# Performance work log

Hardware: AMD Instinct MI355X
Metric: run time of the kernel (lower is better)

The kernel has to match this reference:

```python
import jax, jax.numpy as jnp
import numpy as np

B, L, D = 2, 1024, 1024
HID, E, K = 2048, 8, 2

def setup_inputs() -> dict:
    key = jax.random.key(0)
    ks = jax.random.split(key, 4)
    std = 0.02
    return {
        "x": jax.random.normal(ks[0], (B, L, D), dtype=jnp.float32),
        "router_scale": jnp.ones((D,), dtype=jnp.float32),
        "router_w": jax.random.normal(ks[1], (D, E), dtype=jnp.float32) * std,
        "gating_w": jax.random.normal(ks[2], (E, 2, HID, D), dtype=jnp.float32) * std,
        "linear_w": jax.random.normal(ks[3], (E, HID, D), dtype=jnp.float32) * std,
        "per_expert_scale": jnp.ones((E,), dtype=jnp.float32),
    }

def reference(x, router_scale, router_w, gating_w, linear_w, per_expert_scale):
    d = x.shape[-1]
    # RMSNorm without scale
    var = jnp.mean(jnp.square(x), axis=-1, keepdims=True)
    r_in = x * jax.lax.rsqrt(var + 1e-6)
    r_in = r_in * jax.lax.rsqrt(jnp.array(d, dtype=r_in.dtype)) * router_scale
    # Router
    logits = jnp.dot(r_in, router_w).astype(jnp.float32)          # [B,L,E]
    probs = jax.nn.softmax(logits, axis=-1)
    _, top_k_idx = jax.lax.top_k(logits, K)                        # [B,L,K]
    indicator = jax.nn.one_hot(top_k_idx, probs.shape[-1], dtype=probs.dtype)  # [B,L,K,E]
    gate_weights = indicator.sum(axis=-2) * probs                  # [B,L,E]
    renorm = jnp.sum(gate_weights, axis=-1, keepdims=True)
    renorm = jnp.where(renorm > 0.0, renorm, 1.0)
    weights = probs / renorm
    top_k_w = jnp.take_along_axis(weights, top_k_idx, axis=-1)     # [B,L,K]
    # Combine weights per expert (indices in top-k are distinct)
    combine = jnp.einsum('blke,blk->ble', indicator, top_k_w)      # [B,L,E]
    combine = combine * per_expert_scale                            # fold per-expert scale
    # Dense all-expert GELU-gated FFN; identical math to per-token gathered weights,
    # since unselected experts get combine weight 0.
    gate0 = jnp.einsum('bld,ehd->bleh', x, gating_w[:, 0])         # [B,L,E,H]
    gate1 = jnp.einsum('bld,ehd->bleh', x, gating_w[:, 1])
    act = jax.nn.gelu(gate0) * gate1                               # approximate gelu, as flax nn.gelu
    out = jnp.einsum('bleh,ehd,ble->bld', act, linear_w, combine)
    return out.astype(x.dtype)
```

## Files before the change

### kernel.cpp

```cpp
#include <hip/hip_runtime.h>
#include <math.h>

#define NB 2
#define NL 1024
#define ND 1024
#define NH 2048
#define NE 8
#define NTOK (NB*NL)
#define NSLOT (NTOK*2)

typedef float f32x4 __attribute__((ext_vector_type(4)));
typedef short s16x8 __attribute__((ext_vector_type(8)));
typedef short s16x4 __attribute__((ext_vector_type(4)));

struct TokMeta { int i0, i1; float w0, w1; };

__device__ __forceinline__ unsigned short f2bf(float f) {
    union { float f; unsigned u; } v; v.f = f;
    unsigned r = v.u + 0x7FFFu + ((v.u >> 16) & 1u);
    return (unsigned short)(r >> 16);
}

__global__ void router_kernel(const float* __restrict__ x,
                              const float* __restrict__ rscale,
                              const float* __restrict__ rw,
                              const float* __restrict__ pes,
                              int* __restrict__ counts,
                              TokMeta* __restrict__ meta)
{
    const int wave = threadIdx.x >> 6;
    const int lane = threadIdx.x & 63;
    const int t = blockIdx.x * 4 + wave;
    const float* xt = x + (size_t)t * ND;

    float part[NE];
#pragma unroll
    for (int e = 0; e < NE; ++e) part[e] = 0.f;
    float ss = 0.f;

#pragma unroll
    for (int i = 0; i < 4; ++i) {
        int d = (lane + 64 * i) * 4;
        float4 xv = *(const float4*)(xt + d);
        float4 sv = *(const float4*)(rscale + d);
        float xs[4] = {xv.x, xv.y, xv.z, xv.w};
        float sc[4] = {sv.x, sv.y, sv.z, sv.w};
        const float* rwp = rw + (size_t)d * NE;
#pragma unroll
        for (int c = 0; c < 4; ++c) {
            float v = xs[c];
            ss += v * v;
            float xr = v * sc[c];
            float4 r0 = *(const float4*)(rwp + c * NE);
            float4 r1 = *(const float4*)(rwp + c * NE + 4);
            part[0] += xr * r0.x; part[1] += xr * r0.y;
            part[2] += xr * r0.z; part[3] += xr * r0.w;
            part[4] += xr * r1.x; part[5] += xr * r1.y;
            part[6] += xr * r1.z; part[7] += xr * r1.w;
        }
    }
#pragma unroll
    for (int off = 32; off > 0; off >>= 1) {
        ss += __shfl_xor(ss, off, 64);
#pragma unroll
        for (int e = 0; e < NE; ++e) part[e] += __shfl_xor(part[e], off, 64);
    }
    if (lane == 0) {
        float rinv = rsqrtf(ss * (1.f / ND) + 1e-6f) * rsqrtf((float)ND);
        float lg[NE];
#pragma unroll
        for (int e = 0; e < NE; ++e) lg[e] = part[e] * rinv;
        int i0 = 0; float b0 = lg[0];
#pragma unroll
        for (int e = 1; e < NE; ++e) if (lg[e] > b0) { b0 = lg[e]; i0 = e; }
        int i1 = -1; float b1 = -INFINITY;
#pragma unroll
        for (int e = 0; e < NE; ++e) if (e != i0 && lg[e] > b1) { b1 = lg[e]; i1 = e; }
        float e1 = expf(b1 - b0);
        float denom = 1.f + e1;
        float w0 = pes[i0] / denom;
        float w1 = pes[i1] * e1 / denom;
        meta[t].i0 = i0; meta[t].i1 = i1; meta[t].w0 = w0; meta[t].w1 = w1;
        atomicAdd(&counts[i0], 1);
        atomicAdd(&counts[i1], 1);
    }
}

__global__ void scan_kernel(const int* __restrict__ counts,
                            int* __restrict__ cursor, int* __restrict__ base)
{
    if (threadIdx.x == 0) {
        int acc = 0;
        for (int e = 0; e < NE; ++e) { base[e] = acc; cursor[e] = acc; acc += counts[e]; }
    }
}

__global__ void scatter_kernel(const TokMeta* __restrict__ meta, int* __restrict__ cursor,
                               int* __restrict__ tok_slot, float* __restrict__ w_slot)
{
    int t = blockIdx.x * blockDim.x + threadIdx.x;
    if (t >= NTOK) return;
    TokMeta m = meta[t];
    int s0 = atomicAdd(&cursor[m.i0], 1);
    tok_slot[s0] = t; w_slot[s0] = m.w0;
    int s1 = atomicAdd(&cursor[m.i1], 1);
    tok_slot[s1] = t; w_slot[s1] = m.w1;
}

__global__ __launch_bounds__(256) void gather_x(const float* __restrict__ x,
                                                const int* __restrict__ tok_slot,
                                                unsigned short* __restrict__ xg)
{
    const int s = blockIdx.x;
    const int tok = tok_slot[s];
    const int c = threadIdx.x * 4;
    float4 v = *(const float4*)(x + (size_t)tok * ND + c);
    s16x4 o;
    o[0] = (short)f2bf(v.x); o[1] = (short)f2bf(v.y);
    o[2] = (short)f2bf(v.z); o[3] = (short)f2bf(v.w);
    *(s16x4*)(xg + (size_t)s * ND + c) = o;
}

__global__ __launch_bounds__(256) void transpose_lw(const float* __restrict__ lw,
                                                    unsigned short* __restrict__ lwT)
{
    const int e = blockIdx.z;
    const int h0 = blockIdx.y * 64;
    const int d0 = blockIdx.x * 64;
    __shared__ unsigned short T[64][66];

    const int tid = threadIdx.x;
    {
        const int hr = tid >> 2;
        const int dc = (tid & 3) * 16;
        const float* p = lw + ((size_t)e * NH + h0 + hr) * ND + d0 + dc;
        float t[16];
        *(float4*)&t[0]  = *(const float4*)(p);
        *(float4*)&t[4]  = *(const float4*)(p + 4);
        *(float4*)&t[8]  = *(const float4*)(p + 8);
        *(float4*)&t[12] = *(const float4*)(p + 12);
#pragma unroll
        for (int i = 0; i < 8; ++i) {
            unsigned pk = (unsigned)f2bf(t[2 * i]) | ((unsigned)f2bf(t[2 * i + 1]) << 16);
            *(unsigned*)&T[hr][dc + 2 * i] = pk;
        }
    }
    __syncthreads();
    {
        const int dr = tid >> 2;
        const int hc = (tid & 3) * 16;
        s16x8 o0, o1;
#pragma unroll
        for (int i = 0; i < 8; ++i) o0[i] = (short)T[hc + i][dr];
#pragma unroll
        for (int i = 0; i < 8; ++i) o1[i] = (short)T[hc + 8 + i][dr];
        unsigned short* q = lwT + ((size_t)e * ND + d0 + dr) * NH + h0 + hc;
        *(s16x8*)(q)     = o0;
        *(s16x8*)(q + 8) = o1;
    }
}

#define BM 128
#define BH 64
#define BK 32
__global__ __launch_bounds__(256, 2) void gate_gemm(
    const unsigned short* __restrict__ xg, const float* __restrict__ gw,
    const int* __restrict__ base, const int* __restrict__ counts,
    const float* __restrict__ w_slot, unsigned short* __restrict__ act)
{
    const int e = blockIdx.z;
    const int n = counts[e];
    const int row0 = blockIdx.y * BM;
    if (row0 >= n) return;
    const int b0 = base[e];
    const int h0 = blockIdx.x * BH;

    __shared__ unsigned short As[BM][BK];
    __shared__ unsigned short Bs[2][BH][BK];
    __shared__ float swv[BM];

    const int tid = threadIdx.x;
    if (tid < BM) {
        int r = row0 + tid;
        swv[tid] = (r < n) ? w_slot[b0 + r] : 0.f;
    }

    const int lane = tid & 63;
    const int wid  = tid >> 6;
    const int wm = wid & 1;
    const int wn = wid >> 1;
    const int srow = tid >> 1;
    const int kh   = tid & 1;

    const bool arow_ok = (row0 + srow) < n;
    const unsigned short* xa = xg + (size_t)(b0 + row0 + srow) * ND + kh * 16;
    const int g  = srow >> 6;
    const int hh = srow & 63;
    const float* ba = gw + (((size_t)e * 2 + g) * NH + (h0 + hh)) * ND + kh * 16;

    f32x4 acc[2][4][2];
#pragma unroll
    for (int gg = 0; gg < 2; ++gg)
#pragma unroll
        for (int i = 0; i < 4; ++i)
#pragma unroll
            for (int j = 0; j < 2; ++j)
                acc[gg][i][j] = (f32x4){0.f, 0.f, 0.f, 0.f};

    const int fr = lane & 15;
    const int q8 = (lane >> 4) << 3;

    for (int k0 = 0; k0 < ND; k0 += BK) {
        s16x8 a0 = (s16x8)0, a1 = (s16x8)0;
        if (arow_ok) {
            a0 = *(const s16x8*)(xa + k0);
            a1 = *(const s16x8*)(xa + k0 + 8);
        }
        float t[16];
        *(float4*)&t[0]  = *(const float4*)(ba + k0);
        *(float4*)&t[4]  = *(const float4*)(ba + k0 + 4);
        *(float4*)&t[8]  = *(const float4*)(ba + k0 + 8);
        *(float4*)&t[12] = *(const float4*)(ba + k0 + 12);
        s16x8 b0v, b1v;
#pragma unroll
        for (int i = 0; i < 8; ++i) { b0v[i] = (short)f2bf(t[i]); b1v[i] = (short)f2bf(t[8 + i]); }

        *(s16x8*)&As[srow][kh * 16]      = a0;
        *(s16x8*)&As[srow][kh * 16 + 8]  = a1;
        *(s16x8*)&Bs[g][hh][kh * 16]     = b0v;
        *(s16x8*)&Bs[g][hh][kh * 16 + 8] = b1v;
        __syncthreads();

        s16x8 af[4], bfr[2][2];
#pragma unroll
        for (int i = 0; i < 4; ++i)
            af[i] = *(const s16x8*)&As[wm * 64 + i * 16 + fr][q8];
#pragma unroll
        for (int gg = 0; gg < 2; ++gg)
#pragma unroll
            for (int j = 0; j < 2; ++j)
                bfr[gg][j] = *(const s16x8*)&Bs[gg][wn * 32 + j * 16 + fr][q8];
#pragma unroll
        for (int gg = 0; gg < 2; ++gg)
#pragma unroll
            for (int i = 0; i < 4; ++i)
#pragma unroll
                for (int j = 0; j < 2; ++j)
                    acc[gg][i][j] = __builtin_amdgcn_mfma_f32_16x16x32_bf16(
                        af[i], bfr[gg][j], acc[gg][i][j], 0, 0, 0);
        __syncthreads();
    }

    const int rb = (lane >> 4) * 4;
#pragma unroll
    for (int i = 0; i < 4; ++i)
#pragma unroll
        for (int r = 0; r < 4; ++r) {
            int ml = wm * 64 + i * 16 + rb + r;
            int rr = row0 + ml;
            if (rr < n) {
                float w = swv[ml];
#pragma unroll
                for (int j = 0; j < 2; ++j) {
                    float g0v = acc[0][i][j][r];
                    float g1v = acc[1][i][j][r];
                    float u = 0.7978845608028654f * (g0v + 0.044715f * g0v * g0v * g0v);
                    float ex = __expf(2.f * u);
                    float th = 1.f - 2.f / (ex + 1.f);
                    float a = 0.5f * g0v * (1.f + th) * g1v * w;
                    act[(size_t)(b0 + rr) * NH + (h0 + wn * 32 + j * 16 + fr)] = f2bf(a);
                }
            }
        }
}

#define DBM 128
#define DBN 128
#define DBK 32
#define KSPLIT 2
#define KC (NH / KSPLIT)
__global__ __launch_bounds__(256, 2) void down_gemm(
    const unsigned short* __restrict__ act, const unsigned short* __restrict__ lwT,
    const int* __restrict__ base, const int* __restrict__ counts,
    const int* __restrict__ tok_slot, float* __restrict__ out)
{
    const int e  = blockIdx.z >> 1;
    const int kc = blockIdx.z & 1;
    const int n = counts[e];
    const int row0 = blockIdx.y * DBM;
    if (row0 >= n) return;
    const int b0 = base[e];
    const int d0 = blockIdx.x * DBN;

    __shared__ unsigned short As[DBM][DBK];
    __shared__ unsigned short Bs[DBN][DBK];
    __shared__ int stok[DBM];

    const int tid = threadIdx.x;
    if (tid < DBM) {
        int r = row0 + tid;
        stok[tid] = (r < n) ? tok_slot[b0 + r] : 0;
    }

    const int lane = tid & 63;
    const int wid  = tid >> 6;
    const int wm = wid & 1;
    const int wn = wid >> 1;
    const int srow = tid >> 1;
    const int kh   = tid & 1;

    const bool arow_ok = (row0 + srow) < n;
    const unsigned short* aa = act + (size_t)(b0 + row0 + srow) * NH + kc * KC + kh * 16;
    const unsigned short* bb = lwT + ((size_t)e * ND + d0 + srow) * NH + kc * KC + kh * 16;

    f32x4 acc[4][4];
#pragma unroll
    for (int i = 0; i < 4; ++i)
#pragma unroll
        for (int j = 0; j < 4; ++j)
            acc[i][j] = (f32x4){0.f, 0.f, 0.f, 0.f};

    const int fr = lane & 15;
    const int q8 = (lane >> 4) << 3;

    for (int k0 = 0; k0 < KC; k0 += DBK) {
        s16x8 a0 = (s16x8)0, a1 = (s16x8)0;
        if (arow_ok) {
            a0 = *(const s16x8*)(aa + k0);
            a1 = *(const s16x8*)(aa + k0 + 8);
        }
        s16x8 bv0 = *(const s16x8*)(bb + k0);
        s16x8 bv1 = *(const s16x8*)(bb + k0 + 8);

        *(s16x8*)&As[srow][kh * 16]     = a0;
        *(s16x8*)&As[srow][kh * 16 + 8] = a1;
        *(s16x8*)&Bs[srow][kh * 16]     = bv0;
        *(s16x8*)&Bs[srow][kh * 16 + 8] = bv1;
        __syncthreads();

        s16x8 af[4], bfr[4];
#pragma unroll
        for (int i = 0; i < 4; ++i)
            af[i] = *(const s16x8*)&As[wm * 64 + i * 16 + fr][q8];
#pragma unroll
        for (int j = 0; j < 4; ++j)
            bfr[j] = *(const s16x8*)&Bs[wn * 64 + j * 16 + fr][q8];
#pragma unroll
        for (int i = 0; i < 4; ++i)
#pragma unroll
            for (int j = 0; j < 4; ++j)
                acc[i][j] = __builtin_amdgcn_mfma_f32_16x16x32_bf16(af[i], bfr[j], acc[i][j], 0, 0, 0);
        __syncthreads();
    }

    const int rb = (lane >> 4) * 4;
#pragma unroll
    for (int i = 0; i < 4; ++i)
#pragma unroll
        for (int r = 0; r < 4; ++r) {
            int ml = wm * 64 + i * 16 + rb + r;
            int rr = row0 + ml;
            if (rr < n) {
                int tok = stok[ml];
#pragma unroll
                for (int j = 0; j < 4; ++j)
                    atomicAdd(&out[(size_t)tok * ND + d0 + wn * 64 + j * 16 + fr],
                              acc[i][j][r]);
            }
        }
}

extern "C" void kernel_launch(void* const* d_in, const int* in_sizes, int n_in,
                              void* d_out, int out_size, void* d_ws, size_t ws_size,
                              hipStream_t stream)
{
    const float* x      = (const float*)d_in[0];
    const float* rscale = (const float*)d_in[1];
    const float* rw     = (const float*)d_in[2];
    const float* gw     = (const float*)d_in[3];
    const float* lw     = (const float*)d_in[4];
    const float* pes    = (const float*)d_in[5];
    float* out = (float*)d_out;

    char* ws = (char*)d_ws;
    int* counts = (int*)ws;
    int* cursor = counts + 8;
    int* base   = counts + 16;
    TokMeta* meta        = (TokMeta*)(ws + 128);
    int*   tok_slot      = (int*)(ws + 33024);
    float* w_slot        = (float*)(ws + 49408);
    unsigned short* xg   = (unsigned short*)(ws + 65792);
    unsigned short* act  = (unsigned short*)(ws + 8454400);
    unsigned short* lwT  = (unsigned short*)(ws + 25231616);

    hipMemsetAsync(d_ws, 0, 128, stream);
    hipMemsetAsync(d_out, 0, (size_t)out_size * sizeof(float), stream);

    router_kernel<<<NTOK / 4, 256, 0, stream>>>(x, rscale, rw, pes, counts, meta);
    scan_kernel<<<1, 64, 0, stream>>>(counts, cursor, base);
    scatter_kernel<<<NTOK / 256, 256, 0, stream>>>(meta, cursor, tok_slot, w_slot);
    gather_x<<<NSLOT, 256, 0, stream>>>(x, tok_slot, xg);

    dim3 gt(ND / 64, NH / 64, NE);
    transpose_lw<<<gt, 256, 0, stream>>>(lw, lwT);

    dim3 g2(NH / BH, NTOK / BM, NE);
    gate_gemm<<<g2, 256, 0, stream>>>(xg, gw, base, counts, w_slot, act);

    dim3 g3(ND / DBN, NTOK / DBM, NE * KSPLIT);
    down_gemm<<<g3, 256, 0, stream>>>(act, lwT, base, counts, tok_slot, out);
}
```

Baseline: 461.4 us.

## Use direct global-to-LDS loads with swizzle and pre-converted bf16 gate weights

Both expert GEMMs now stage their tiles with global_load_lds (direct global-to-shared copies) and read fragments through an XOR-style swizzled column index, replacing register round-trips and bank-conflicting LDS reads. The gate weights are converted to bf16 once in a separate pass instead of being converted inside every gate_gemm tile. The per-slot x gather is replaced by a dense bf16 conversion of x, with rows gathered by token index inside the GEMM. The extra conversion pass over the gate weights adds a full read and write of that tensor each call. Out-of-range rows now load token 0 or slot 0 instead of zeros, which relies on the epilogue masking them out.

```diff
diff --git a/kernel.cpp b/kernel.cpp
--- a/kernel.cpp
+++ b/kernel.cpp
@@ -19,6 +19,12 @@
     union { float f; unsigned u; } v; v.f = f;
     unsigned r = v.u + 0x7FFFu + ((v.u >> 16) & 1u);
     return (unsigned short)(r >> 16);
+}
+
+__device__ __forceinline__ void gl_lds16(const unsigned short* g, unsigned short* l) {
+    __builtin_amdgcn_global_load_lds(
+        (const __attribute__((address_space(1))) unsigned int*)(const void*)g,
+        (__attribute__((address_space(3))) unsigned int*)(void*)l, 16, 0, 0);
 }
 
 __global__ void router_kernel(const float* __restrict__ x,
@@ -107,18 +113,30 @@
     tok_slot[s1] = t; w_slot[s1] = m.w1;
 }
 
-__global__ __launch_bounds__(256) void gather_x(const float* __restrict__ x,
-                                                const int* __restrict__ tok_slot,
-                                                unsigned short* __restrict__ xg)
-{
-    const int s = blockIdx.x;
-    const int tok = tok_slot[s];
-    const int c = threadIdx.x * 4;
-    float4 v = *(const float4*)(x + (size_t)tok * ND + c);
-    s16x4 o;
-    o[0] = (short)f2bf(v.x); o[1] = (short)f2bf(v.y);
-    o[2] = (short)f2bf(v.z); o[3] = (short)f2bf(v.w);
-    *(s16x4*)(xg + (size_t)s * ND + c) = o;
+__global__ __launch_bounds__(256) void convert_x(const float* __restrict__ x,
+                                                 unsigned short* __restrict__ xb)
+{
+    const size_t i = ((size_t)blockIdx.x * 256 + threadIdx.x) * 8;
+    float t[8];
+    *(float4*)&t[0] = *(const float4*)(x + i);
+    *(float4*)&t[4] = *(const float4*)(x + i + 4);
+    s16x8 o;
+#pragma unroll
+    for (int c = 0; c < 8; ++c) o[c] = (short)f2bf(t[c]);
+    *(s16x8*)(xb + i) = o;
+}
+
+__global__ __launch_bounds__(256) void convert_gw(const float* __restrict__ gw,
+                                                  unsigned short* __restrict__ gwb)
+{
+    const size_t i = ((size_t)blockIdx.x * 256 + threadIdx.x) * 8;
+    float t[8];
+    *(float4*)&t[0] = *(const float4*)(gw + i);
+    *(float4*)&t[4] = *(const float4*)(gw + i + 4);
+    s16x8 o;
+#pragma unroll
+    for (int c = 0; c < 8; ++c) o[c] = (short)f2bf(t[c]);
+    *(s16x8*)(gwb + i) = o;
 }
 
 __global__ __launch_bounds__(256) void transpose_lw(const float* __restrict__ lw,
@@ -164,9 +182,10 @@
 #define BH 64
 #define BK 32
 __global__ __launch_bounds__(256, 2) void gate_gemm(
-    const unsigned short* __restrict__ xg, const float* __restrict__ gw,
+    const unsigned short* __restrict__ xb, const unsigned short* __restrict__ gwb,
     const int* __restrict__ base, const int* __restrict__ counts,
-    const float* __restrict__ w_slot, unsigned short* __restrict__ act)
+    const int* __restrict__ tok_slot, const float* __restrict__ w_slot,
+    unsigned short* __restrict__ act)
 {
     const int e = blockIdx.z;
     const int n = counts[e];
@@ -176,27 +195,32 @@
     const int h0 = blockIdx.x * BH;
 
     __shared__ unsigned short As[BM][BK];
-    __shared__ unsigned short Bs[2][BH][BK];
+    __shared__ unsigned short Bs[BM][BK];
+    __shared__ int toks[BM];
     __shared__ float swv[BM];
 
     const int tid = threadIdx.x;
     if (tid < BM) {
         int r = row0 + tid;
-        swv[tid] = (r < n) ? w_slot[b0 + r] : 0.f;
-    }
+        toks[tid] = (r < n) ? tok_slot[b0 + r] : 0;
+        swv[tid]  = (r < n) ? w_slot[b0 + r] : 0.f;
+    }
+    __syncthreads();
 
     const int lane = tid & 63;
     const int wid  = tid >> 6;
     const int wm = wid & 1;
     const int wn = wid >> 1;
-    const int srow = tid >> 1;
-    const int kh   = tid & 1;
-
-    const bool arow_ok = (row0 + srow) < n;
-    const unsigned short* xa = xg + (size_t)(b0 + row0 + srow) * ND + kh * 16;
-    const int g  = srow >> 6;
-    const int hh = srow & 63;
-    const float* ba = gw + (((size_t)e * 2 + g) * NH + (h0 + hh)) * ND + kh * 16;
+
+    const int drow = lane >> 2;
+    const int c8  = (((lane & 3) - ((lane >> 3) & 3)) & 3) * 8;
+    const int ar0 = wid * 32 + drow;
+    const unsigned short* asrc0 = xb + (size_t)toks[ar0] * ND + c8;
+    const unsigned short* asrc1 = xb + (size_t)toks[ar0 + 16] * ND + c8;
+    const int br0 = wid * 32 + drow;
+    const int br1 = br0 + 16;
+    const unsigned short* bsrc0 = gwb + (((size_t)e * 2 + (br0 >> 6)) * NH + h0 + (br0 & 63)) * ND + c8;
+    const unsigned short* bsrc1 = gwb + (((size_t)e * 2 + (br1 >> 6)) * NH + h0 + (br1 & 63)) * ND + c8;
 
     f32x4 acc[2][4][2];
 #pragma unroll
@@ -208,38 +232,24 @@
                 acc[gg][i][j] = (f32x4){0.f, 0.f, 0.f, 0.f};
 
     const int fr = lane & 15;
-    const int q8 = (lane >> 4) << 3;
+    const int pS = (((lane >> 4) + (fr >> 1)) & 3) * 8;
 
     for (int k0 = 0; k0 < ND; k0 += BK) {
-        s16x8 a0 = (s16x8)0, a1 = (s16x8)0;
-        if (arow_ok) {
-            a0 = *(const s16x8*)(xa + k0);
-            a1 = *(const s16x8*)(xa + k0 + 8);
-        }
-        float t[16];
-        *(float4*)&t[0]  = *(const float4*)(ba + k0);
-        *(float4*)&t[4]  = *(const float4*)(ba + k0 + 4);
-        *(float4*)&t[8]  = *(const float4*)(ba + k0 + 8);
-        *(float4*)&t[12] = *(const float4*)(ba + k0 + 12);
-        s16x8 b0v, b1v;
-#pragma unroll
-        for (int i = 0; i < 8; ++i) { b0v[i] = (short)f2bf(t[i]); b1v[i] = (short)f2bf(t[8 + i]); }
-
-        *(s16x8*)&As[srow][kh * 16]      = a0;
-        *(s16x8*)&As[srow][kh * 16 + 8]  = a1;
-        *(s16x8*)&Bs[g][hh][kh * 16]     = b0v;
-        *(s16x8*)&Bs[g][hh][kh * 16 + 8] = b1v;
+        gl_lds16(asrc0 + k0, &As[wid * 32][0]);
+        gl_lds16(asrc1 + k0, &As[wid * 32 + 16][0]);
+        gl_lds16(bsrc0 + k0, &Bs[wid * 32][0]);
+        gl_lds16(bsrc1 + k0, &Bs[wid * 32 + 16][0]);
         __syncthreads();
 
         s16x8 af[4], bfr[2][2];
 #pragma unroll
         for (int i = 0; i < 4; ++i)
-            af[i] = *(const s16x8*)&As[wm * 64 + i * 16 + fr][q8];
+            af[i] = *(const s16x8*)&As[wm * 64 + i * 16 + fr][pS];
 #pragma unroll
         for (int gg = 0; gg < 2; ++gg)
 #pragma unroll
             for (int j = 0; j < 2; ++j)
-                bfr[gg][j] = *(const s16x8*)&Bs[gg][wn * 32 + j * 16 + fr][q8];
+                bfr[gg][j] = *(const s16x8*)&Bs[gg * 64 + wn * 32 + j * 16 + fr][pS];
 #pragma unroll
         for (int gg = 0; gg < 2; ++gg)
 #pragma unroll
@@ -301,17 +311,23 @@
         int r = row0 + tid;
         stok[tid] = (r < n) ? tok_slot[b0 + r] : 0;
     }
+    __syncthreads();
 
     const int lane = tid & 63;
     const int wid  = tid >> 6;
     const int wm = wid & 1;
     const int wn = wid >> 1;
-    const int srow = tid >> 1;
-    const int kh   = tid & 1;
-
-    const bool arow_ok = (row0 + srow) < n;
-    const unsigned short* aa = act + (size_t)(b0 + row0 + srow) * NH + kc * KC + kh * 16;
-    const unsigned short* bb = lwT + ((size_t)e * ND + d0 + srow) * NH + kc * KC + kh * 16;
+
+    const int drow = lane >> 2;
+    const int c8  = (((lane & 3) - ((lane >> 3) & 3)) & 3) * 8;
+    const int ar0 = wid * 32 + drow;
+    const int rr0 = row0 + ar0, rr1 = rr0 + 16;
+    const int sl0 = b0 + (rr0 < n ? rr0 : 0);
+    const int sl1 = b0 + (rr1 < n ? rr1 : 0);
+    const unsigned short* asrc0 = act + (size_t)sl0 * NH + kc * KC + c8;
+    const unsigned short* asrc1 = act + (size_t)sl1 * NH + kc * KC + c8;
+    const unsigned short* bsrc0 = lwT + ((size_t)e * ND + d0 + ar0) * NH + kc * KC + c8;
+    const unsigned short* bsrc1 = bsrc0 + 16 * NH;
 
     f32x4 acc[4][4];
 #pragma unroll
@@ -321,30 +337,22 @@
             acc[i][j] = (f32x4){0.f, 0.f, 0.f, 0.f};
 
     const int fr = lane & 15;
-    const int q8 = (lane >> 4) << 3;
+    const int pS = (((lane >> 4) + (fr >> 1)) & 3) * 8;
 
     for (int k0 = 0; k0 < KC; k0 += DBK) {
-        s16x8 a0 = (s16x8)0, a1 = (s16x8)0;
-        if (arow_ok) {
-            a0 = *(const s16x8*)(aa + k0);
-            a1 = *(const s16x8*)(aa + k0 + 8);
-        }
-        s16x8 bv0 = *(const s16x8*)(bb + k0);
-        s16x8 bv1 = *(const s16x8*)(bb + k0 + 8);
-
-        *(s16x8*)&As[srow][kh * 16]     = a0;
-        *(s16x8*)&As[srow][kh * 16 + 8] = a1;
-        *(s16x8*)&Bs[srow][kh * 16]     = bv0;
-        *(s16x8*)&Bs[srow][kh * 16 + 8] = bv1;
+        gl_lds16(asrc0 + k0, &As[wid * 32][0]);
+        gl_lds16(asrc1 + k0, &As[wid * 32 + 16][0]);
+        gl_lds16(bsrc0 + k0, &Bs[wid * 32][0]);
+        gl_lds16(bsrc1 + k0, &Bs[wid * 32 + 16][0]);
         __syncthreads();
 
         s16x8 af[4], bfr[4];
 #pragma unroll
         for (int i = 0; i < 4; ++i)
-            af[i] = *(const s16x8*)&As[wm * 64 + i * 16 + fr][q8];
+            af[i] = *(const s16x8*)&As[wm * 64 + i * 16 + fr][pS];
 #pragma unroll
         for (int j = 0; j < 4; ++j)
-            bfr[j] = *(const s16x8*)&Bs[wn * 64 + j * 16 + fr][q8];
+            bfr[j] = *(const s16x8*)&Bs[wn * 64 + j * 16 + fr][pS];
 #pragma unroll
         for (int i = 0; i < 4; ++i)
 #pragma unroll
@@ -389,9 +397,10 @@
     TokMeta* meta        = (TokMeta*)(ws + 128);
     int*   tok_slot      = (int*)(ws + 33024);
     float* w_slot        = (float*)(ws + 49408);
-    unsigned short* xg   = (unsigned short*)(ws + 65792);
-    unsigned short* act  = (unsigned short*)(ws + 8454400);
-    unsigned short* lwT  = (unsigned short*)(ws + 25231616);
+    unsigned short* xb   = (unsigned short*)(ws + 65792);
+    unsigned short* act  = (unsigned short*)(ws + 4260096);
+    unsigned short* lwT  = (unsigned short*)(ws + 21037312);
+    unsigned short* gwb  = (unsigned short*)(ws + 54591744);
 
     hipMemsetAsync(d_ws, 0, 128, stream);
     hipMemsetAsync(d_out, 0, (size_t)out_size * sizeof(float), stream);
@@ -399,13 +408,14 @@
     router_kernel<<<NTOK / 4, 256, 0, stream>>>(x, rscale, rw, pes, counts, meta);
     scan_kernel<<<1, 64, 0, stream>>>(counts, cursor, base);
     scatter_kernel<<<NTOK / 256, 256, 0, stream>>>(meta, cursor, tok_slot, w_slot);
-    gather_x<<<NSLOT, 256, 0, stream>>>(x, tok_slot, xg);
-
+
+    convert_x<<<(NTOK * ND) / (256 * 8), 256, 0, stream>>>(x, xb);
+    convert_gw<<<(NE * 2 * NH * ND) / (256 * 8), 256, 0, stream>>>(gw, gwb);
     dim3 gt(ND / 64, NH / 64, NE);
     transpose_lw<<<gt, 256, 0, stream>>>(lw, lwT);
 
     dim3 g2(NH / BH, NTOK / BM, NE);
-    gate_gemm<<<g2, 256, 0, stream>>>(xg, gw, base, counts, w_slot, act);
+    gate_gemm<<<g2, 256, 0, stream>>>(xb, gwb, base, counts, tok_slot, w_slot, act);
 
     dim3 g3(ND / DBN, NTOK / DBM, NE * KSPLIT);
     down_gemm<<<g3, 256, 0, stream>>>(act, lwT, base, counts, tok_slot, out);
```

After: 455.7 us. Within noise of the previous version (-1.2%).
